# Optimization experiments

Hardware: AMD Instinct MI355X
Metric: run time of the kernel (lower is better)

Reference implementation:

```python
import jax, jax.numpy as jnp
import numpy as np

EPS = np.finfo(np.float32).eps
X_DIM, H_DIM, Z_DIM = 256, 1024, 128
T, B = 128, 256

def _lin(key, fan_in, fan_out):
    k1, k2 = jax.random.split(key)
    lim = 1.0 / np.sqrt(fan_in)
    W = jax.random.uniform(k1, (fan_in, fan_out), jnp.float32, -lim, lim)
    b = jax.random.uniform(k2, (fan_out,), jnp.float32, -lim, lim)
    return W, b

def setup_inputs() -> dict:
    key = jax.random.key(0)
    ks = jax.random.split(key, 20)
    inp = {}
    inp['x'] = jax.random.normal(ks[0], (T, B, X_DIM), jnp.float32)
    inp['h'] = jnp.zeros((1, B, H_DIM), jnp.float32)
    inp['eps'] = jax.random.normal(ks[1], (T, B, Z_DIM), jnp.float32)
    inp['Wpx'], inp['bpx'] = _lin(ks[2], X_DIM, H_DIM)
    inp['Wpz'], inp['bpz'] = _lin(ks[3], Z_DIM, H_DIM)
    inp['Wenc'], inp['benc'] = _lin(ks[4], 2 * H_DIM, H_DIM)
    inp['Wem'], inp['bem'] = _lin(ks[5], H_DIM, Z_DIM)
    inp['Wes'], inp['bes'] = _lin(ks[6], H_DIM, Z_DIM)
    inp['Wpr'], inp['bpr'] = _lin(ks[7], H_DIM, H_DIM)
    inp['Wpm'], inp['bpm'] = _lin(ks[8], H_DIM, Z_DIM)
    inp['Wps'], inp['bps'] = _lin(ks[9], H_DIM, Z_DIM)
    inp['Wdec'], inp['bdec'] = _lin(ks[10], 2 * H_DIM, H_DIM)
    inp['Wdm'], inp['bdm'] = _lin(ks[11], H_DIM, X_DIM)
    inp['Wds'], inp['bds'] = _lin(ks[12], H_DIM, X_DIM)
    # GRU (pytorch layout): W_ih [3H, 2H], W_hh [3H, H]
    lim = 1.0 / np.sqrt(H_DIM)
    inp['W_ih'] = jax.random.uniform(ks[13], (3 * H_DIM, 2 * H_DIM), jnp.float32, -lim, lim)
    inp['W_hh'] = jax.random.uniform(ks[14], (3 * H_DIM, H_DIM), jnp.float32, -lim, lim)
    inp['b_ih'] = jax.random.uniform(ks[15], (3 * H_DIM,), jnp.float32, -lim, lim)
    inp['b_hh'] = jax.random.uniform(ks[16], (3 * H_DIM,), jnp.float32, -lim, lim)
    return inp

def reference(x, h, eps, Wpx, bpx, Wpz, bpz, Wenc, benc, Wem, bem, Wes, bes,
              Wpr, bpr, Wpm, bpm, Wps, bps, Wdec, bdec, Wdm, bdm, Wds, bds,
              W_ih, W_hh, b_ih, b_hh):
    relu = jax.nn.relu
    sp = jax.nn.softplus

    def gru_cell(inp, h_prev):
        gi = inp @ W_ih.T + b_ih          # [B, 3H]
        gh = h_prev @ W_hh.T + b_hh       # [B, 3H]
        i_r, i_z, i_n = jnp.split(gi, 3, axis=-1)
        h_r, h_z, h_n = jnp.split(gh, 3, axis=-1)
        r = jax.nn.sigmoid(i_r + h_r)
        u = jax.nn.sigmoid(i_z + h_z)
        n = jnp.tanh(i_n + r * h_n)
        return (1.0 - u) * n + u * h_prev

    def step(h_t, xe):
        x_t, eps_t = xe
        phi_x_t = relu(x_t @ Wpx + bpx)                               # [B,H]
        enc_t = relu(jnp.concatenate([phi_x_t, h_t], axis=1) @ Wenc + benc)
        enc_mean_t = enc_t @ Wem + bem
        enc_std_t = sp(enc_t @ Wes + bes)
        z_t = enc_mean_t + eps_t * enc_std_t                          # reparam
        phi_z_t = relu(z_t @ Wpz + bpz)
        prior_t = relu(h_t @ Wpr + bpr)
        prior_mean_t = prior_t @ Wpm + bpm
        prior_std_t = sp(prior_t @ Wps + bps)
        dec_t = relu(jnp.concatenate([phi_z_t, h_t], axis=1) @ Wdec + bdec)
        dec_mean_t = dec_t @ Wdm + bdm
        dec_std_t = sp(dec_t @ Wds + bds)
        h_next = gru_cell(jnp.concatenate([phi_x_t, phi_z_t], axis=1), h_t)
        kld_t = 0.5 * jnp.sum(2.0 * jnp.log(prior_std_t + EPS) - 2.0 * jnp.log(enc_std_t + EPS)
                              + (enc_std_t ** 2 + (enc_mean_t - prior_mean_t) ** 2) / prior_std_t ** 2 - 1.0)
        nll_t = jnp.sum(jnp.log(dec_std_t + EPS) + 0.5 * jnp.log(2.0 * jnp.pi)
                        + (x_t - dec_mean_t) ** 2 / (2.0 * dec_std_t ** 2))
        return h_next, (enc_mean_t, enc_std_t, dec_mean_t, dec_std_t, kld_t, nll_t)

    h0 = h[0]  # [B, H]
    _, (enc_means, enc_stds, dec_means, dec_stds, klds, nlls) = jax.lax.scan(step, h0, (x, eps))
    kld_loss = jnp.sum(klds)
    nll_loss = jnp.sum(nlls)
    return (kld_loss, nll_loss, enc_means, enc_stds, dec_means, dec_stds)
```

## Files before the change

kernel.cpp:

```cpp
#include <hip/hip_runtime.h>
#include <math.h>
#include <limits.h>

#define T_DIM 128
#define B_DIM 256
#define X_DIMC 256
#define H_DIMC 1024
#define Z_DIMC 128
#define EPSF 1.1920929e-07f
#define HALF_LOG_2PI 0.91893853320467274f
#define NBLK 768
#define NPB (NBLK / 64)
#define BARN ((66 + 64) * 32)

typedef float f32x4 __attribute__((ext_vector_type(4)));
typedef short bf16x8 __attribute__((ext_vector_type(8)));

struct Seg { int n_end; int kbeg; int kend; const float* bias; int act;
             float* of32; int ld32; short* ob16; int ld16; };
struct Segs { Seg s[4]; };

__host__ __device__ static inline Seg dseg(int n_end, int kbeg, int kend,
    const float* bias, int act, float* of32, int ld32, short* ob16, int ld16)
{
    Seg s; s.n_end = n_end; s.kbeg = kbeg; s.kend = kend; s.bias = bias;
    s.act = act; s.of32 = of32; s.ld32 = ld32; s.ob16 = ob16; s.ld16 = ld16;
    return s;
}
__host__ __device__ static inline Seg dsegend()
{ return dseg(INT_MAX, 0, 64, nullptr, 0, nullptr, 0, nullptr, 0); }

__device__ __forceinline__ short f2bf(float f) {
    unsigned u = __builtin_bit_cast(unsigned, f);
    u += 0x7fffu + ((u >> 16) & 1u);
    return (short)(u >> 16);
}
__device__ __forceinline__ float act_apply(float x, int act) {
    if (act == 1) return fmaxf(x, 0.f);
    if (act == 2) return x > 0.f ? x + log1pf(expf(-x)) : log1pf(expf(x));
    return x;
}
__device__ __forceinline__ void gload16(const short* g, short* l) {
    __builtin_amdgcn_global_load_lds(
        (const __attribute__((address_space(1))) void*)g,
        (__attribute__((address_space(3))) void*)l, 16, 0, 0);
}
__device__ __forceinline__ void gload16a(const short* g, short* l) {
    __builtin_amdgcn_global_load_lds(
        (const __attribute__((address_space(1))) void*)g,
        (__attribute__((address_space(3))) void*)l, 16, 0, 17);
}
__device__ __forceinline__ float ldf(const float* p) {
    return __hip_atomic_load(p, __ATOMIC_RELAXED, __HIP_MEMORY_SCOPE_AGENT);
}
__device__ __forceinline__ void stf(float* p, float v) {
    __hip_atomic_store(p, v, __ATOMIC_RELAXED, __HIP_MEMORY_SCOPE_AGENT);
}
__device__ __forceinline__ void sth(short* p, short v) {
    __hip_atomic_store(p, v, __ATOMIC_RELAXED, __HIP_MEMORY_SCOPE_AGENT);
}

__device__ __forceinline__ void gridbar(unsigned* bar, int phase) {
    __syncthreads();
    if (threadIdx.x == 0) {
        asm volatile("s_waitcnt vmcnt(0) lgkmcnt(0)" ::: "memory");
        const int leaf = blockIdx.x & 63;
        unsigned* leafc = bar + (leaf << 5);
        unsigned* rootc = bar + (64 << 5);
        unsigned* rgen  = bar + (65 << 5);
        unsigned* lgen  = bar + ((66 + leaf) << 5);
        unsigned old = __hip_atomic_fetch_add(leafc, 1u, __ATOMIC_RELAXED,
                                              __HIP_MEMORY_SCOPE_AGENT);
        if (((old + 1u) % (unsigned)NPB) == 0u) {
            unsigned r = __hip_atomic_fetch_add(rootc, 1u, __ATOMIC_RELAXED,
                                                __HIP_MEMORY_SCOPE_AGENT);
            if (((r + 1u) & 63u) == 0u)
                __hip_atomic_store(rgen, (r + 1u) >> 6, __ATOMIC_RELAXED,
                                   __HIP_MEMORY_SCOPE_AGENT);
            unsigned g; int it = 0;
            while ((int)(g = __hip_atomic_load(rgen, __ATOMIC_RELAXED,
                                               __HIP_MEMORY_SCOPE_AGENT)) < phase) {
                if (it < 4) { __builtin_amdgcn_s_sleep(1); ++it; }
                else        { __builtin_amdgcn_s_sleep(8); }
            }
            __hip_atomic_store(lgen, g, __ATOMIC_RELAXED,
                               __HIP_MEMORY_SCOPE_AGENT);
        } else {
            int it = 0;
            while ((int)__hip_atomic_load(lgen, __ATOMIC_RELAXED,
                                          __HIP_MEMORY_SCOPE_AGENT) < phase) {
                if (it < 4) { __builtin_amdgcn_s_sleep(1); ++it; }
                else        { __builtin_amdgcn_s_sleep(8); }
            }
        }
    }
    __syncthreads();
}

__device__ __forceinline__ void gemm_tile(
    short* __restrict__ smem, int bm0, int bn0,
    const short* __restrict__ A0, int lda0,
    const short* __restrict__ A1, int lda1,
    const short* __restrict__ A2, int lda2,
    int ks1, int ks2,
    const short* __restrict__ BT, int ldb, const Segs& segs)
{
    short* As = smem;
    short* Bs = smem + 12288;
    const int tid = threadIdx.x, lane = tid & 63, wid = tid >> 6;
    __syncthreads();
    Seg sg; int n0;
    if      (bn0 < segs.s[0].n_end) { sg = segs.s[0]; n0 = 0; }
    else if (bn0 < segs.s[1].n_end) { sg = segs.s[1]; n0 = segs.s[0].n_end; }
    else if (bn0 < segs.s[2].n_end) { sg = segs.s[2]; n0 = segs.s[1].n_end; }
    else                            { sg = segs.s[3]; n0 = segs.s[2].n_end; }
    const int nit = (sg.kend - sg.kbeg) >> 6;
    const int row8 = lane >> 3;
    const int kc = ((lane & 7) ^ row8) << 3;
    const int r0 = (wid << 4) + row8, r1 = r0 + 8;

    auto srcA = [&](int r, int gk) -> const short* {
        return (gk < ks1) ? A0 + (size_t)(bm0 + r) * lda0 + gk
             : (gk < ks2) ? A1 + (size_t)(bm0 + r) * lda1 + (gk - ks1)
                          : A2 + (size_t)(bm0 + r) * lda2 + (gk - ks2);
    };
    auto stage = [&](int p, int it) {
        const int gk = sg.kbeg + (it << 6) + kc;
        gload16a(srcA(r0, gk), As + p * 4096 + ((wid << 4) + 0) * 64);
        gload16a(srcA(r1, gk), As + p * 4096 + ((wid << 4) + 8) * 64);
        gload16(BT + (size_t)(bn0 + r0) * ldb + gk, Bs + p * 4096 + ((wid << 4) + 0) * 64);
        gload16(BT + (size_t)(bn0 + r1) * ldb + gk, Bs + p * 4096 + ((wid << 4) + 8) * 64);
    };

    const int l15 = lane & 15, lg = lane >> 4;
    const int wm = (wid >> 1) << 5, wn = (wid & 1) << 5;
    const int swz = (l15 & 7) << 3;
    const int c0 = (lg << 3) ^ swz;
    const int c1 = (32 + (lg << 3)) ^ swz;
    f32x4 acc[2][2] = {};

    stage(0, 0);
    if (nit > 1) stage(1, 1);
    if (nit > 2) stage(2, 2);
    int p = 0;
    for (int it = 0; it < nit; ++it) {
        const int rem = nit - 1 - it;
        if (rem >= 2)      asm volatile("s_waitcnt vmcnt(8)" ::: "memory");
        else if (rem == 1) asm volatile("s_waitcnt vmcnt(4)" ::: "memory");
        else               asm volatile("s_waitcnt vmcnt(0)" ::: "memory");
        asm volatile("s_barrier" ::: "memory");
        const short* Ap = As + p * 4096;
        const short* Bp = Bs + p * 4096;
        bf16x8 a00 = *(const bf16x8*)(Ap + (wm + l15) * 64 + c0);
        bf16x8 a01 = *(const bf16x8*)(Ap + (wm + l15) * 64 + c1);
        bf16x8 a10 = *(const bf16x8*)(Ap + (wm + 16 + l15) * 64 + c0);
        bf16x8 a11 = *(const bf16x8*)(Ap + (wm + 16 + l15) * 64 + c1);
        bf16x8 b00 = *(const bf16x8*)(Bp + (wn + l15) * 64 + c0);
        bf16x8 b01 = *(const bf16x8*)(Bp + (wn + l15) * 64 + c1);
        bf16x8 b10 = *(const bf16x8*)(Bp + (wn + 16 + l15) * 64 + c0);
        bf16x8 b11 = *(const bf16x8*)(Bp + (wn + 16 + l15) * 64 + c1);
        acc[0][0] = __builtin_amdgcn_mfma_f32_16x16x32_bf16(a00, b00, acc[0][0], 0, 0, 0);
        acc[0][1] = __builtin_amdgcn_mfma_f32_16x16x32_bf16(a00, b10, acc[0][1], 0, 0, 0);
        acc[1][0] = __builtin_amdgcn_mfma_f32_16x16x32_bf16(a10, b00, acc[1][0], 0, 0, 0);
        acc[1][1] = __builtin_amdgcn_mfma_f32_16x16x32_bf16(a10, b10, acc[1][1], 0, 0, 0);
        acc[0][0] = __builtin_amdgcn_mfma_f32_16x16x32_bf16(a01, b01, acc[0][0], 0, 0, 0);
        acc[0][1] = __builtin_amdgcn_mfma_f32_16x16x32_bf16(a01, b11, acc[0][1], 0, 0, 0);
        acc[1][0] = __builtin_amdgcn_mfma_f32_16x16x32_bf16(a11, b01, acc[1][0], 0, 0, 0);
        acc[1][1] = __builtin_amdgcn_mfma_f32_16x16x32_bf16(a11, b11, acc[1][1], 0, 0, 0);
        if (rem >= 3) {
            asm volatile("s_waitcnt lgkmcnt(0)\n\ts_barrier" ::: "memory");
            stage(p, it + 3);
        }
        p = (p == 2) ? 0 : p + 1;
    }

#pragma unroll
    for (int j = 0; j < 2; ++j) {
        const int gn = bn0 + wn + (j << 4) + l15;
        const int cn = gn - n0;
        const float bv = sg.bias[cn];
#pragma unroll
        for (int i = 0; i < 2; ++i) {
            const int gm0 = bm0 + wm + (i << 4) + (lg << 2);
#pragma unroll
            for (int r = 0; r < 4; ++r) {
                float v = act_apply(acc[i][j][r] + bv, sg.act);
                if (sg.of32) stf(sg.of32 + (size_t)(gm0 + r) * sg.ld32 + cn, v);
                if (sg.ob16) sth(sg.ob16 + (size_t)(gm0 + r) * sg.ld16 + cn, f2bf(v));
            }
        }
    }
}

__device__ __forceinline__ void z_tile(
    short* __restrict__ smem, int bm0, int bn0,
    const float* __restrict__ zm, const float* __restrict__ zs,
    const float* __restrict__ ze,
    const short* __restrict__ BT, const float* __restrict__ bias,
    short* __restrict__ outb)
{
    short* Az = smem;
    short* Bz = smem + 64 * 136;
    const int tid = threadIdx.x, lane = tid & 63, wid = tid >> 6;
    __syncthreads();
    const int r = tid >> 2, c0i = (tid & 3) << 3;
#pragma unroll
    for (int s = 0; s < 4; ++s) {
        const int col = c0i + s * 32;
        const size_t base = (size_t)(bm0 + r) * 128 + col;
        short tmp[8];
#pragma unroll
        for (int q = 0; q < 8; ++q) {
            const float m = ldf(zm + base + q);
            const float sd = ldf(zs + base + q);
            const float e = ze[base + q];
            tmp[q] = f2bf(fmaf(e, sd, m));
        }
        *(bf16x8*)(Az + r * 136 + col) = *(bf16x8*)tmp;
        *(bf16x8*)(Bz + r * 136 + col) =
            *(const bf16x8*)(BT + (size_t)(bn0 + r) * 128 + col);
    }
    __syncthreads();
    const int l15 = lane & 15, lg = lane >> 4;
    const int wm = (wid >> 1) << 5, wn = (wid & 1) << 5;
    f32x4 acc[2][2] = {};
#pragma unroll
    for (int s = 0; s < 4; ++s) {
        bf16x8 af0 = *(const bf16x8*)(Az + (wm + l15) * 136 + (lg << 3) + s * 32);
        bf16x8 af1 = *(const bf16x8*)(Az + (wm + 16 + l15) * 136 + (lg << 3) + s * 32);
        bf16x8 bg0 = *(const bf16x8*)(Bz + (wn + l15) * 136 + (lg << 3) + s * 32);
        bf16x8 bg1 = *(const bf16x8*)(Bz + (wn + 16 + l15) * 136 + (lg << 3) + s * 32);
        acc[0][0] = __builtin_amdgcn_mfma_f32_16x16x32_bf16(af0, bg0, acc[0][0], 0, 0, 0);
        acc[0][1] = __builtin_amdgcn_mfma_f32_16x16x32_bf16(af0, bg1, acc[0][1], 0, 0, 0);
        acc[1][0] = __builtin_amdgcn_mfma_f32_16x16x32_bf16(af1, bg0, acc[1][0], 0, 0, 0);
        acc[1][1] = __builtin_amdgcn_mfma_f32_16x16x32_bf16(af1, bg1, acc[1][1], 0, 0, 0);
    }
#pragma unroll
    for (int j = 0; j < 2; ++j) {
        const int gn = bn0 + wn + (j << 4) + l15;
        const float bv = bias[gn];
#pragma unroll
        for (int i = 0; i < 2; ++i) {
            const int gm0 = bm0 + wm + (i << 4) + (lg << 2);
#pragma unroll
            for (int rr = 0; rr < 4; ++rr) {
                float v = fmaxf(acc[i][j][rr] + bv, 0.f);
                sth(outb + (size_t)(gm0 + rr) * 1024 + gn, f2bf(v));
            }
        }
    }
}

__device__ __forceinline__ void gru_unit(int uid, int tid,
    const float* __restrict__ gi, const float* __restrict__ gh,
    const float* __restrict__ h, float* __restrict__ hn, short* __restrict__ hnb)
{
    const int i = uid * 256 + tid;
    const int b = i >> 10, j = i & (H_DIMC - 1);
    const float* gib = gi + (size_t)b * 3 * H_DIMC;
    const float* ghb = gh + (size_t)b * 3 * H_DIMC;
    const float r = 1.f / (1.f + expf(-(ldf(gib + j) + ldf(ghb + j))));
    const float u = 1.f / (1.f + expf(-(ldf(gib + H_DIMC + j) + ldf(ghb + H_DIMC + j))));
    const float n = tanhf(ldf(gib + 2 * H_DIMC + j) + r * ldf(ghb + 2 * H_DIMC + j));
    const float v = (1.f - u) * n + u * ldf(h + i);
    stf(hn + i, v); sth(hnb + i, f2bf(v));
}

__device__ __forceinline__ void loss_unit(int uid, int tid,
    const float* __restrict__ em, const float* __restrict__ es,
    const float* __restrict__ pm, const float* __restrict__ ps,
    const float* __restrict__ xt, const float* __restrict__ dm,
    const float* __restrict__ ds, float* __restrict__ outp, float* sred)
{
    const int KB = (B_DIM * Z_DIMC) / 256;
    float v; int target;
    if (uid < KB) {
        const int i = uid * 256 + tid;
        const float esv = ldf(es + i), psv = ldf(ps + i);
        const float dmn = ldf(em + i) - ldf(pm + i);
        v = 0.5f * (2.f * logf(psv + EPSF) - 2.f * logf(esv + EPSF) +
                    (esv * esv + dmn * dmn) / (psv * psv) - 1.f);
        target = 0;
    } else {
        const int i = (uid - KB) * 256 + tid;
        const float d = ldf(ds + i);
        const float diff = xt[i] - ldf(dm + i);
        v = logf(d + EPSF) + HALF_LOG_2PI + diff * diff / (2.f * d * d);
        target = 1;
    }
    for (int o = 32; o > 0; o >>= 1) v += __shfl_down(v, o);
    if ((tid & 63) == 0) sred[tid >> 6] = v;
    __syncthreads();
    if (tid == 0) atomicAdd(outp + target, sred[0] + sred[1] + sred[2] + sred[3]);
    __syncthreads();
}

struct PP {
    const short* xb; const float* x; const float* eps;
    const short *WTpx, *WT1, *WT2, *WTpz, *WT4, *WT56;
    const float *bpx, *benc, *bpr, *bhh, *bem, *bes, *bpz, *bdec, *bih,
                *bpm, *bps, *bdm, *bds;
    float *hf0, *hf1; short *hb0, *hb1;
    short *enc_b, *prior_b, *phi_zb, *dec_b;
    short *phiXb, *phiXs;
    float *ghb, *gib, *pmb, *psb;
    float *kld, *em, *es, *dm, *ds;
    unsigned* bar; int big;
};

__global__ __launch_bounds__(256, 3) void vrnn_k(PP p)
{
    __shared__ short smem[24576];
    __shared__ float sred[4];
    const int G = gridDim.x, bid = blockIdx.x, tid = threadIdx.x;
    const int BIGK = 1 << 30;
    int ph = 0;

    Segs sx;
    sx.s[0] = dseg(1024, 0, 256, p.bpx, 1, nullptr, 0, p.big ? p.phiXb : p.phiXs, 1024);
    sx.s[1] = dsegend(); sx.s[2] = dsegend(); sx.s[3] = dsegend();

    if (p.big) {
        for (int u = bid; u < 512 * 16; u += G)
            gemm_tile(smem, (u & 511) << 6, (u >> 9) << 6,
                      p.xb, 256, p.xb, 256, p.xb, 256, BIGK, BIGK,
                      p.WTpx, 256, sx);
        gridbar(p.bar, ++ph);
    }

    for (int t = 0; t < T_DIM; ++t) {
        float* hcur = (t & 1) ? p.hf1 : p.hf0;
        float* hnxt = (t & 1) ? p.hf0 : p.hf1;
        const short* hbc = (t & 1) ? p.hb1 : p.hb0;
        short* hbn = (t & 1) ? p.hb0 : p.hb1;
        const short* phiXt = p.big ? p.phiXb + (size_t)t * B_DIM * H_DIMC : p.phiXs;
        float* em_t = p.em + (size_t)t * B_DIM * Z_DIMC;
        float* es_t = p.es + (size_t)t * B_DIM * Z_DIMC;
        float* dm_t = p.dm + (size_t)t * B_DIM * X_DIMC;
        float* ds_t = p.ds + (size_t)t * B_DIM * X_DIMC;
        const float* eps_t = p.eps + (size_t)t * B_DIM * Z_DIMC;

        if (!p.big) {
            for (int u = bid; u < 64; u += G)
                gemm_tile(smem, (u & 3) << 6, (u >> 2) << 6,
                          p.xb + (size_t)t * B_DIM * X_DIMC, 256,
                          p.xb, 256, p.xb, 256, BIGK, BIGK, p.WTpx, 256, sx);
            gridbar(p.bar, ++ph);
        }
        {
            Segs g1;
            g1.s[0] = dseg(1024, 0, 2048, p.benc, 1, nullptr, 0, p.enc_b, 1024);
            g1.s[1] = dseg(2048, 1024, 2048, p.bpr, 1, nullptr, 0, p.prior_b, 1024);
            g1.s[2] = dseg(5120, 1024, 2048, p.bhh, 0, p.ghb, 3 * H_DIMC, nullptr, 0);
            g1.s[3] = dsegend();
            const int tp = t - 1;
            const int nA = 320 + (t > 0 ? 384 : 0);
            for (int u = bid; u < nA; u += G) {
                if (u < 320)
                    gemm_tile(smem, (u & 3) << 6, (u >> 2) << 6,
                              phiXt, 1024, hbc, 1024, hbc, 1024, 1024, BIGK,
                              p.WT1, 2048, g1);
                else
                    loss_unit(u - 320, tid,
                              p.em + (size_t)tp * B_DIM * Z_DIMC,
                              p.es + (size_t)tp * B_DIM * Z_DIMC,
                              p.pmb, p.psb,
                              p.x + (size_t)tp * B_DIM * X_DIMC,
                              p.dm + (size_t)tp * B_DIM * X_DIMC,
                              p.ds + (size_t)tp * B_DIM * X_DIMC,
                              p.kld, sred);
            }
            gridbar(p.bar, ++ph);
        }
        {
            Segs g2;
            g2.s[0] = dseg(128, 0, 1024, p.bem, 0, em_t, 128, nullptr, 0);
            g2.s[1] = dseg(256, 0, 1024, p.bes, 2, es_t, 128, nullptr, 0);
            g2.s[2] = dsegend(); g2.s[3] = dsegend();
            for (int u = bid; u < 16; u += G)
                gemm_tile(smem, (u & 3) << 6, (u >> 2) << 6,
                          p.enc_b, 1024, p.enc_b, 1024, p.enc_b, 1024, BIGK, BIGK,
                          p.WT2, 1024, g2);
            gridbar(p.bar, ++ph);
        }
        for (int u = bid; u < 64; u += G)
            z_tile(smem, (u & 3) << 6, (u >> 2) << 6,
                   em_t, es_t, eps_t, p.WTpz, p.bpz, p.phi_zb);
        gridbar(p.bar, ++ph);
        {
            Segs g4;
            g4.s[0] = dseg(1024, 1024, 3072, p.bdec, 1, nullptr, 0, p.dec_b, 1024);
            g4.s[1] = dseg(4096, 0, 2048, p.bih, 0, p.gib, 3 * H_DIMC, nullptr, 0);
            g4.s[2] = dsegend(); g4.s[3] = dsegend();
            for (int u = bid; u < 256; u += G)
                gemm_tile(smem, (u & 3) << 6, (u >> 2) << 6,
                          phiXt, 1024, p.phi_zb, 1024, hbc, 1024, 1024, 2048,
                          p.WT4, 3072, g4);
            gridbar(p.bar, ++ph);
        }
        {
            Segs g5;
            g5.s[0] = dseg(128, 0, 1024, p.bpm, 0, p.pmb, 128, nullptr, 0);
            g5.s[1] = dseg(256, 0, 1024, p.bps, 2, p.psb, 128, nullptr, 0);
            g5.s[2] = dseg(512, 1024, 2048, p.bdm, 0, dm_t, 256, nullptr, 0);
            g5.s[3] = dseg(768, 1024, 2048, p.bds, 2, ds_t, 256, nullptr, 0);
            for (int u = bid; u < 48 + 1024; u += G) {
                if (u < 48)
                    gemm_tile(smem, (u & 3) << 6, (u >> 2) << 6,
                              p.prior_b, 1024, p.dec_b, 1024, p.dec_b, 1024,
                              1024, BIGK, p.WT56, 2048, g5);
                else
                    gru_unit(u - 48, tid, p.gib, p.ghb, hcur, hnxt, hbn);
            }
            gridbar(p.bar, ++ph);
        }
    }
    {
        const int tp = T_DIM - 1;
        for (int u = bid; u < 384; u += G)
            loss_unit(u, tid,
                      p.em + (size_t)tp * B_DIM * Z_DIMC,
                      p.es + (size_t)tp * B_DIM * Z_DIMC,
                      p.pmb, p.psb,
                      p.x + (size_t)tp * B_DIM * X_DIMC,
                      p.dm + (size_t)tp * B_DIM * X_DIMC,
                      p.ds + (size_t)tp * B_DIM * X_DIMC,
                      p.kld, sred);
    }
}

__global__ void packT_k(const float* __restrict__ src, int ldsr,
                        short* __restrict__ dst, int ldd, int n0, int k0)
{
    __shared__ float tile[32][33];
    const int bx = blockIdx.x * 32, by = blockIdx.y * 32;
    const int tx = threadIdx.x, ty = threadIdx.y;
    for (int i = ty; i < 32; i += 8)
        tile[i][tx] = src[(size_t)(by + i) * ldsr + bx + tx];
    __syncthreads();
    for (int i = ty; i < 32; i += 8)
        dst[(size_t)(n0 + bx + i) * ldd + k0 + by + tx] = f2bf(tile[tx][i]);
}

__global__ void packD_k(const float* __restrict__ src, int ldsr,
                        short* __restrict__ dst, int ldd, int n0, int k0, int kr)
{
    const int idx = blockIdx.x * 256 + threadIdx.x;
    const int n = idx / kr, k = idx % kr;
    dst[(size_t)(n0 + n) * ldd + k0 + k] = f2bf(src[(size_t)n * ldsr + k]);
}

__global__ void cvtx_k(const float* __restrict__ x, short* __restrict__ xb)
{
    const int i = blockIdx.x * 256 + threadIdx.x;
    float4 v = ((const float4*)x)[i];
    short4 s;
    s.x = f2bf(v.x); s.y = f2bf(v.y); s.z = f2bf(v.z); s.w = f2bf(v.w);
    ((short4*)xb)[i] = s;
}

__global__ void hinit_k(const float* __restrict__ h0, float* __restrict__ hf,
                        short* __restrict__ hb)
{
    const int i = blockIdx.x * 256 + threadIdx.x;
    const float v = h0[i];
    hf[i] = v; hb[i] = f2bf(v);
}

__global__ void init_k(unsigned* bar, float* kn)
{
    for (int i = threadIdx.x; i < BARN; i += 256) bar[i] = 0u;
    if (threadIdx.x < 2) kn[threadIdx.x] = 0.f;
}

extern "C" void kernel_launch(void* const* d_in, const int* in_sizes, int n_in,
                              void* d_out_v, int out_size, void* d_ws, size_t ws_size,
                              hipStream_t stream)
{
    (void)in_sizes; (void)n_in; (void)out_size;
    const float* x    = (const float*)d_in[0];
    const float* h0   = (const float*)d_in[1];
    const float* eps  = (const float*)d_in[2];
    const float* Wpx  = (const float*)d_in[3];
    const float* bpx  = (const float*)d_in[4];
    const float* Wpz  = (const float*)d_in[5];
    const float* bpz  = (const float*)d_in[6];
    const float* Wenc = (const float*)d_in[7];
    const float* benc = (const float*)d_in[8];
    const float* Wem  = (const float*)d_in[9];
    const float* bem  = (const float*)d_in[10];
    const float* Wes  = (const float*)d_in[11];
    const float* bes  = (const float*)d_in[12];
    const float* Wpr  = (const float*)d_in[13];
    const float* bpr  = (const float*)d_in[14];
    const float* Wpm  = (const float*)d_in[15];
    const float* bpm  = (const float*)d_in[16];
    const float* Wps  = (const float*)d_in[17];
    const float* bps  = (const float*)d_in[18];
    const float* Wdec = (const float*)d_in[19];
    const float* bdec = (const float*)d_in[20];
    const float* Wdm  = (const float*)d_in[21];
    const float* bdm  = (const float*)d_in[22];
    const float* Wds  = (const float*)d_in[23];
    const float* bds  = (const float*)d_in[24];
    const float* W_ih = (const float*)d_in[25];
    const float* W_hh = (const float*)d_in[26];
    const float* b_ih = (const float*)d_in[27];
    const float* b_hh = (const float*)d_in[28];

    float* out = (float*)d_out_v;

    char* wsb = (char*)d_ws;
    size_t off = 0;
    auto takeB = [&](size_t bytes) {
        char* p = wsb + off; off += (bytes + 255) & ~(size_t)255; return p;
    };
    short* WTpx = (short*)takeB((size_t)1024 * 256 * 2);
    short* WT1  = (short*)takeB((size_t)5120 * 2048 * 2);
    short* WT2  = (short*)takeB((size_t)256 * 1024 * 2);
    short* WTpz = (short*)takeB((size_t)1024 * 128 * 2);
    short* WT4  = (short*)takeB((size_t)4096 * 3072 * 2);
    short* WT56 = (short*)takeB((size_t)768 * 2048 * 2);
    short* xb   = (short*)takeB((size_t)T_DIM * B_DIM * X_DIMC * 2);
    float* hf0  = (float*)takeB((size_t)B_DIM * H_DIMC * 4);
    float* hf1  = (float*)takeB((size_t)B_DIM * H_DIMC * 4);
    short* hb0  = (short*)takeB((size_t)B_DIM * H_DIMC * 2);
    short* hb1  = (short*)takeB((size_t)B_DIM * H_DIMC * 2);
    short* enc_b   = (short*)takeB((size_t)B_DIM * H_DIMC * 2);
    short* prior_b = (short*)takeB((size_t)B_DIM * H_DIMC * 2);
    short* phi_zb  = (short*)takeB((size_t)B_DIM * H_DIMC * 2);
    short* dec_b   = (short*)takeB((size_t)B_DIM * H_DIMC * 2);
    float* ghb_ = (float*)takeB((size_t)B_DIM * 3 * H_DIMC * 4);
    float* gib_ = (float*)takeB((size_t)B_DIM * 3 * H_DIMC * 4);
    float* pmb  = (float*)takeB((size_t)B_DIM * Z_DIMC * 4);
    float* psb  = (float*)takeB((size_t)B_DIM * Z_DIMC * 4);
    unsigned* bar = (unsigned*)takeB((size_t)BARN * 4);
    const size_t phiXb_bytes = (size_t)T_DIM * B_DIM * H_DIMC * 2;
    const bool big = (off + phiXb_bytes) <= ws_size;
    short* phiXb = big ? (short*)takeB(phiXb_bytes) : nullptr;
    short* phiXs = big ? nullptr : (short*)takeB((size_t)B_DIM * H_DIMC * 2);

    const dim3 tb(256), pt(32, 8);

    packT_k<<<dim3(32, 8), pt, 0, stream>>>(Wpx, 1024, WTpx, 256, 0, 0);
    packT_k<<<dim3(32, 64), pt, 0, stream>>>(Wenc, 1024, WT1, 2048, 0, 0);
    packT_k<<<dim3(32, 32), pt, 0, stream>>>(Wpr, 1024, WT1, 2048, 1024, 1024);
    packD_k<<<dim3(3072 * 1024 / 256), tb, 0, stream>>>(W_hh, 1024, WT1, 2048, 2048, 1024, 1024);
    packT_k<<<dim3(4, 32), pt, 0, stream>>>(Wem, 128, WT2, 1024, 0, 0);
    packT_k<<<dim3(4, 32), pt, 0, stream>>>(Wes, 128, WT2, 1024, 128, 0);
    packT_k<<<dim3(32, 4), pt, 0, stream>>>(Wpz, 1024, WTpz, 128, 0, 0);
    packT_k<<<dim3(32, 64), pt, 0, stream>>>(Wdec, 1024, WT4, 3072, 0, 1024);
    packD_k<<<dim3(3072 * 2048 / 256), tb, 0, stream>>>(W_ih, 2048, WT4, 3072, 1024, 0, 2048);
    packT_k<<<dim3(4, 32), pt, 0, stream>>>(Wpm, 128, WT56, 2048, 0, 0);
    packT_k<<<dim3(4, 32), pt, 0, stream>>>(Wps, 128, WT56, 2048, 128, 0);
    packT_k<<<dim3(8, 32), pt, 0, stream>>>(Wdm, 256, WT56, 2048, 256, 1024);
    packT_k<<<dim3(8, 32), pt, 0, stream>>>(Wds, 256, WT56, 2048, 512, 1024);

    cvtx_k<<<dim3((size_t)T_DIM * B_DIM * X_DIMC / 4 / 256), tb, 0, stream>>>(x, xb);
    hinit_k<<<dim3(B_DIM * H_DIMC / 256), tb, 0, stream>>>(h0, hf0, hb0);
    init_k<<<1, 256, 0, stream>>>(bar, out);

    PP p;
    p.xb = xb; p.x = x; p.eps = eps;
    p.WTpx = WTpx; p.WT1 = WT1; p.WT2 = WT2; p.WTpz = WTpz; p.WT4 = WT4; p.WT56 = WT56;
    p.bpx = bpx; p.benc = benc; p.bpr = bpr; p.bhh = b_hh; p.bem = bem; p.bes = bes;
    p.bpz = bpz; p.bdec = bdec; p.bih = b_ih; p.bpm = bpm; p.bps = bps;
    p.bdm = bdm; p.bds = bds;
    p.hf0 = hf0; p.hf1 = hf1; p.hb0 = hb0; p.hb1 = hb1;
    p.enc_b = enc_b; p.prior_b = prior_b; p.phi_zb = phi_zb; p.dec_b = dec_b;
    p.phiXb = phiXb; p.phiXs = phiXs;
    p.ghb = ghb_; p.gib = gib_; p.pmb = pmb; p.psb = psb;
    p.kld = out; p.em = out + 2;
    p.es = p.em + (size_t)T_DIM * B_DIM * Z_DIMC;
    p.dm = p.es + (size_t)T_DIM * B_DIM * Z_DIMC;
    p.ds = p.dm + (size_t)T_DIM * B_DIM * X_DIMC;
    p.bar = bar; p.big = big ? 1 : 0;

    vrnn_k<<<dim3(NBLK), tb, 0, stream>>>(p);
}
```

Baseline: 15.54 ms.

## Deepen GEMM pipeline to six stages with 32-wide K slices and cached A loads

The GEMM tile loop now uses K slices of 32 instead of 64, with a 6-deep LDS ring instead of 3-deep. The staging layout and swizzle are reworked so that each lane loads one row chunk for A and one for B. A new flag lets A0 loads use the cached load path when the operand is read-only (phiX/x) instead of the always-fresh variant. The aim is more loads in flight and lower latency per barrier, at the cost of twice as many barriers and iterations per tile.

```diff
diff --git a/kernel.cpp b/kernel.cpp
--- a/kernel.cpp
+++ b/kernel.cpp
@@ -102,7 +102,7 @@
     const short* __restrict__ A0, int lda0,
     const short* __restrict__ A1, int lda1,
     const short* __restrict__ A2, int lda2,
-    int ks1, int ks2,
+    int ks1, int ks2, int a0c,
     const short* __restrict__ BT, int ldb, const Segs& segs)
 {
     short* As = smem;
@@ -114,64 +114,58 @@
     else if (bn0 < segs.s[1].n_end) { sg = segs.s[1]; n0 = segs.s[0].n_end; }
     else if (bn0 < segs.s[2].n_end) { sg = segs.s[2]; n0 = segs.s[1].n_end; }
     else                            { sg = segs.s[3]; n0 = segs.s[2].n_end; }
-    const int nit = (sg.kend - sg.kbeg) >> 6;
-    const int row8 = lane >> 3;
-    const int kc = ((lane & 7) ^ row8) << 3;
-    const int r0 = (wid << 4) + row8, r1 = r0 + 8;
-
-    auto srcA = [&](int r, int gk) -> const short* {
-        return (gk < ks1) ? A0 + (size_t)(bm0 + r) * lda0 + gk
-             : (gk < ks2) ? A1 + (size_t)(bm0 + r) * lda1 + (gk - ks1)
-                          : A2 + (size_t)(bm0 + r) * lda2 + (gk - ks2);
+    const int nit = (sg.kend - sg.kbeg) >> 5;
+    const int row16 = lane >> 2;
+    const int kc = ((lane & 3) ^ ((lane >> 3) & 3)) << 3;
+    const int r0 = (wid << 4) + row16;
+
+    auto srcA = [&](int gk) -> const short* {
+        return (gk < ks1) ? A0 + (size_t)(bm0 + r0) * lda0 + gk
+             : (gk < ks2) ? A1 + (size_t)(bm0 + r0) * lda1 + (gk - ks1)
+                          : A2 + (size_t)(bm0 + r0) * lda2 + (gk - ks2);
     };
     auto stage = [&](int p, int it) {
-        const int gk = sg.kbeg + (it << 6) + kc;
-        gload16a(srcA(r0, gk), As + p * 4096 + ((wid << 4) + 0) * 64);
-        gload16a(srcA(r1, gk), As + p * 4096 + ((wid << 4) + 8) * 64);
-        gload16(BT + (size_t)(bn0 + r0) * ldb + gk, Bs + p * 4096 + ((wid << 4) + 0) * 64);
-        gload16(BT + (size_t)(bn0 + r1) * ldb + gk, Bs + p * 4096 + ((wid << 4) + 8) * 64);
+        const int gk = sg.kbeg + (it << 5) + kc;
+        short* dA = As + p * 2048 + (wid << 9);
+        short* dB = Bs + p * 2048 + (wid << 9);
+        const short* ga = srcA(gk);
+        if (a0c && gk < ks1) gload16(ga, dA);
+        else                 gload16a(ga, dA);
+        gload16(BT + (size_t)(bn0 + r0) * ldb + gk, dB);
     };
 
     const int l15 = lane & 15, lg = lane >> 4;
     const int wm = (wid >> 1) << 5, wn = (wid & 1) << 5;
-    const int swz = (l15 & 7) << 3;
-    const int c0 = (lg << 3) ^ swz;
-    const int c1 = (32 + (lg << 3)) ^ swz;
+    const int co = (lg ^ ((l15 >> 1) & 3)) << 3;
     f32x4 acc[2][2] = {};
 
-    stage(0, 0);
-    if (nit > 1) stage(1, 1);
-    if (nit > 2) stage(2, 2);
+#pragma unroll
+    for (int i = 0; i < 6; ++i) if (i < nit) stage(i, i);
     int p = 0;
     for (int it = 0; it < nit; ++it) {
         const int rem = nit - 1 - it;
-        if (rem >= 2)      asm volatile("s_waitcnt vmcnt(8)" ::: "memory");
-        else if (rem == 1) asm volatile("s_waitcnt vmcnt(4)" ::: "memory");
+        if      (rem >= 5) asm volatile("s_waitcnt vmcnt(10)" ::: "memory");
+        else if (rem == 4) asm volatile("s_waitcnt vmcnt(8)" ::: "memory");
+        else if (rem == 3) asm volatile("s_waitcnt vmcnt(6)" ::: "memory");
+        else if (rem == 2) asm volatile("s_waitcnt vmcnt(4)" ::: "memory");
+        else if (rem == 1) asm volatile("s_waitcnt vmcnt(2)" ::: "memory");
         else               asm volatile("s_waitcnt vmcnt(0)" ::: "memory");
         asm volatile("s_barrier" ::: "memory");
-        const short* Ap = As + p * 4096;
-        const short* Bp = Bs + p * 4096;
-        bf16x8 a00 = *(const bf16x8*)(Ap + (wm + l15) * 64 + c0);
-        bf16x8 a01 = *(const bf16x8*)(Ap + (wm + l15) * 64 + c1);
-        bf16x8 a10 = *(const bf16x8*)(Ap + (wm + 16 + l15) * 64 + c0);
-        bf16x8 a11 = *(const bf16x8*)(Ap + (wm + 16 + l15) * 64 + c1);
-        bf16x8 b00 = *(const bf16x8*)(Bp + (wn + l15) * 64 + c0);
-        bf16x8 b01 = *(const bf16x8*)(Bp + (wn + l15) * 64 + c1);
-        bf16x8 b10 = *(const bf16x8*)(Bp + (wn + 16 + l15) * 64 + c0);
-        bf16x8 b11 = *(const bf16x8*)(Bp + (wn + 16 + l15) * 64 + c1);
-        acc[0][0] = __builtin_amdgcn_mfma_f32_16x16x32_bf16(a00, b00, acc[0][0], 0, 0, 0);
-        acc[0][1] = __builtin_amdgcn_mfma_f32_16x16x32_bf16(a00, b10, acc[0][1], 0, 0, 0);
-        acc[1][0] = __builtin_amdgcn_mfma_f32_16x16x32_bf16(a10, b00, acc[1][0], 0, 0, 0);
-        acc[1][1] = __builtin_amdgcn_mfma_f32_16x16x32_bf16(a10, b10, acc[1][1], 0, 0, 0);
-        acc[0][0] = __builtin_amdgcn_mfma_f32_16x16x32_bf16(a01, b01, acc[0][0], 0, 0, 0);
-        acc[0][1] = __builtin_amdgcn_mfma_f32_16x16x32_bf16(a01, b11, acc[0][1], 0, 0, 0);
-        acc[1][0] = __builtin_amdgcn_mfma_f32_16x16x32_bf16(a11, b01, acc[1][0], 0, 0, 0);
-        acc[1][1] = __builtin_amdgcn_mfma_f32_16x16x32_bf16(a11, b11, acc[1][1], 0, 0, 0);
-        if (rem >= 3) {
+        const short* Ap = As + p * 2048;
+        const short* Bp = Bs + p * 2048;
+        bf16x8 a0 = *(const bf16x8*)(Ap + (wm + l15) * 32 + co);
+        bf16x8 a1 = *(const bf16x8*)(Ap + (wm + 16 + l15) * 32 + co);
+        bf16x8 b0 = *(const bf16x8*)(Bp + (wn + l15) * 32 + co);
+        bf16x8 b1 = *(const bf16x8*)(Bp + (wn + 16 + l15) * 32 + co);
+        acc[0][0] = __builtin_amdgcn_mfma_f32_16x16x32_bf16(a0, b0, acc[0][0], 0, 0, 0);
+        acc[0][1] = __builtin_amdgcn_mfma_f32_16x16x32_bf16(a0, b1, acc[0][1], 0, 0, 0);
+        acc[1][0] = __builtin_amdgcn_mfma_f32_16x16x32_bf16(a1, b0, acc[1][0], 0, 0, 0);
+        acc[1][1] = __builtin_amdgcn_mfma_f32_16x16x32_bf16(a1, b1, acc[1][1], 0, 0, 0);
+        if (rem >= 6) {
             asm volatile("s_waitcnt lgkmcnt(0)\n\ts_barrier" ::: "memory");
-            stage(p, it + 3);
-        }
-        p = (p == 2) ? 0 : p + 1;
+            stage(p, it + 6);
+        }
+        p = (p == 5) ? 0 : p + 1;
     }
 
 #pragma unroll
@@ -323,7 +317,7 @@
     if (p.big) {
         for (int u = bid; u < 512 * 16; u += G)
             gemm_tile(smem, (u & 511) << 6, (u >> 9) << 6,
-                      p.xb, 256, p.xb, 256, p.xb, 256, BIGK, BIGK,
+                      p.xb, 256, p.xb, 256, p.xb, 256, BIGK, BIGK, 1,
                       p.WTpx, 256, sx);
         gridbar(p.bar, ++ph);
     }
@@ -344,7 +338,7 @@
             for (int u = bid; u < 64; u += G)
                 gemm_tile(smem, (u & 3) << 6, (u >> 2) << 6,
                           p.xb + (size_t)t * B_DIM * X_DIMC, 256,
-                          p.xb, 256, p.xb, 256, BIGK, BIGK, p.WTpx, 256, sx);
+                          p.xb, 256, p.xb, 256, BIGK, BIGK, 1, p.WTpx, 256, sx);
             gridbar(p.bar, ++ph);
         }
         {
@@ -358,7 +352,7 @@
             for (int u = bid; u < nA; u += G) {
                 if (u < 320)
                     gemm_tile(smem, (u & 3) << 6, (u >> 2) << 6,
-                              phiXt, 1024, hbc, 1024, hbc, 1024, 1024, BIGK,
+                              phiXt, 1024, hbc, 1024, hbc, 1024, 1024, BIGK, 1,
                               p.WT1, 2048, g1);
                 else
                     loss_unit(u - 320, tid,
@@ -379,7 +373,7 @@
             g2.s[2] = dsegend(); g2.s[3] = dsegend();
             for (int u = bid; u < 16; u += G)
                 gemm_tile(smem, (u & 3) << 6, (u >> 2) << 6,
-                          p.enc_b, 1024, p.enc_b, 1024, p.enc_b, 1024, BIGK, BIGK,
+                          p.enc_b, 1024, p.enc_b, 1024, p.enc_b, 1024, BIGK, BIGK, 0,
                           p.WT2, 1024, g2);
             gridbar(p.bar, ++ph);
         }
@@ -394,7 +388,7 @@
             g4.s[2] = dsegend(); g4.s[3] = dsegend();
             for (int u = bid; u < 256; u += G)
                 gemm_tile(smem, (u & 3) << 6, (u >> 2) << 6,
-                          phiXt, 1024, p.phi_zb, 1024, hbc, 1024, 1024, 2048,
+                          phiXt, 1024, p.phi_zb, 1024, hbc, 1024, 1024, 2048, 1,
                           p.WT4, 3072, g4);
             gridbar(p.bar, ++ph);
         }
@@ -408,7 +402,7 @@
                 if (u < 48)
                     gemm_tile(smem, (u & 3) << 6, (u >> 2) << 6,
                               p.prior_b, 1024, p.dec_b, 1024, p.dec_b, 1024,
-                              1024, BIGK, p.WT56, 2048, g5);
+                              1024, BIGK, 0, p.WT56, 2048, g5);
                 else
                     gru_unit(u - 48, tid, p.gib, p.ghb, hcur, hnxt, hbn);
             }
```

New measurement: 15.27 ms. No clear change (-1.8%).
